# Performance work log

Measured on AMD Instinct MI355X. Metric: run time of the kernel, lower is better.

## Reference

```python
import jax, jax.numpy as jnp
import numpy as np
from jax import lax

C = 31  # channels (hyperspectral bands)
DN = ('NCHW', 'OIHW', 'NCHW')


def ln_bias(x, w, b):
    # WithBias LayerNorm over channel dim (torch does it in (b,hw,c) layout)
    mu = x.mean(axis=1, keepdims=True)
    var = x.var(axis=1, keepdims=True)
    xn = (x - mu) * lax.rsqrt(var + 1e-5)
    return xn * w[None, :, None, None] + b[None, :, None, None]


def conv1x1(x, W, b):
    y = lax.conv_general_dilated(x, W, (1, 1), 'VALID', dimension_numbers=DN)
    return y + b[None, :, None, None]


def dwconv3(x, W, b=None):
    c = x.shape[1]
    y = lax.conv_general_dilated(x, W, (1, 1), ((1, 1), (1, 1)),
                                 dimension_numbers=DN, feature_group_count=c)
    if b is not None:
        y = y + b[None, :, None, None]
    return y


def l2norm_lastdim(v):
    n = jnp.sqrt(jnp.sum(v * v, axis=-1, keepdims=True))
    return v / jnp.maximum(n, 1e-12)


def setup_inputs() -> dict:
    key = jax.random.key(0)
    ks = jax.random.split(key, 16)
    B, H, W = 4, 512, 512
    s = 0.05
    d = {
        'x': jax.random.normal(ks[0], (B, 1, H, W), jnp.float32),
        'z': jax.random.normal(ks[1], (B, C, H, W), jnp.float32),
        'nx_w': jnp.ones((1,), jnp.float32),
        'nx_b': jnp.zeros((1,), jnp.float32),
        'nz_w': jnp.ones((C,), jnp.float32),
        'nz_b': jnp.zeros((C,), jnp.float32),
        't1_w': jax.random.normal(ks[2], (C, C, 1, 1), jnp.float32) * s,
        't1_b': jnp.zeros((C,), jnp.float32),
        't2_w': jax.random.normal(ks[3], (C, 1, 3, 3), jnp.float32) * s,
        't2_b': jnp.zeros((C,), jnp.float32),
        'p1_w': jax.random.normal(ks[4], (C, 1, 1, 1), jnp.float32) * s,
        'p1_b': jnp.zeros((C,), jnp.float32),
        'p2_w': jax.random.normal(ks[5], (C, 1, 3, 3), jnp.float32) * s,
        'p2_b': jnp.zeros((C,), jnp.float32),
        'g1_w': jax.random.normal(ks[6], (C, C, 1, 1), jnp.float32) * s,
        'g1_b': jnp.zeros((C,), jnp.float32),
        'g2_w': jax.random.normal(ks[7], (C, 1, 3, 3), jnp.float32) * s,
        'g2_b': jnp.zeros((C,), jnp.float32),
        'w_w': jax.random.normal(ks[8], (C, C, 1, 1), jnp.float32) * s,
        'w_b': jnp.zeros((C,), jnp.float32),
        'v_w': jax.random.normal(ks[9], (C + 1, C + 1, 1, 1), jnp.float32) * s,
        'v_b': jnp.zeros((C + 1,), jnp.float32),
        'pe1_w': jax.random.normal(ks[10], (C, 1, 3, 3), jnp.float32) * s,
        'pe2_w': jax.random.normal(ks[11], (C, 1, 3, 3), jnp.float32) * s,
    }
    return d


def reference(x, z, nx_w, nx_b, nz_w, nz_b, t1_w, t1_b, t2_w, t2_b,
              p1_w, p1_b, p2_w, p2_b, g1_w, g1_b, g2_w, g2_b,
              w_w, w_b, v_w, v_b, pe1_w, pe2_w):
    b, _, h, w = x.shape
    x0 = ln_bias(x, nx_w, nx_b)            # (b,1,h,w)
    z0 = ln_bias(z, nz_w, nz_b)            # (b,C,h,w)

    z1 = dwconv3(conv1x1(z0, t1_w, t1_b), t2_w, t2_b).reshape(b, C, h * w)
    x1 = dwconv3(conv1x1(x0, p1_w, p1_b), p2_w, p2_b).reshape(b, C, h * w)

    z1 = l2norm_lastdim(z1)
    x1 = l2norm_lastdim(x1)

    att = jax.nn.softmax(jnp.einsum('bcn,bdn->bcd', z1, x1), axis=-1)  # (b,C,C)

    z2 = dwconv3(conv1x1(z0, g1_w, g1_b), g2_w, g2_b)  # (b,C,h,w)
    z_v = z2.reshape(b, C, h * w)
    out_x = jnp.einsum('bcd,bdn->bcn', att, z_v).reshape(b, C, h, w)

    pos = dwconv3(jax.nn.gelu(dwconv3(z2, pe1_w), approximate=False), pe2_w)
    out_x = conv1x1(out_x, w_w, w_b) + pos + z

    y = conv1x1(jnp.concatenate([x, out_x], axis=1), v_w, v_b)  # (b,C+1,h,w)
    return y
```

## Files before the change

kernel.cpp:

```cpp
#include <hip/hip_runtime.h>
#include <hip/hip_fp16.h>
#include <math.h>

#define BN 4
#define CC 31
#define HH 512
#define WW 512
#define HWSZ 262144

static const size_t Z2F = (size_t)BN * CC * HWSZ;
#define T_OFF   0
#define SSQ_OFF 124
#define R0_OFF  248
#define RL_OFF  372
#define C0_OFF  496
#define CL_OFF  620
#define COR_OFF 744
#define M2_OFF  1240
#define VB2_OFF 5208

typedef short v8s __attribute__((ext_vector_type(8)));
typedef _Float16 v8h __attribute__((ext_vector_type(8)));
typedef float v4f __attribute__((ext_vector_type(4)));
typedef _Float16 v4h __attribute__((ext_vector_type(4)));

__device__ __forceinline__ short f2bf(float f) {
    unsigned u = __float_as_uint(f);
    return (short)((u + 0x7FFFu + ((u >> 16) & 1u)) >> 16);
}

__device__ __forceinline__ float fast_gelu(float s) {
    const float a  = fabsf(s) * 0.70710678118654752f;
    const float t  = __builtin_amdgcn_rcpf(1.f + 0.3275911f * a);
    float p = 1.061405429f;
    p = p * t - 1.453152027f;
    p = p * t + 1.421413741f;
    p = p * t - 0.284496736f;
    p = p * t + 0.254829592f;
    const float e  = __expf(-a * a);
    const float er = copysignf(1.f - p * t * e, s);
    return 0.5f * s * (1.f + er);
}

__device__ __forceinline__ void swizzle_tile(int& b, int& ty0, int& tx0) {
    const int lid = blockIdx.x + 32 * blockIdx.y + 1024 * blockIdx.z;
    const int vid = ((lid & 7) << 9) + (lid >> 3);
    b = vid >> 10;
    const int rem = vid & 1023;
    ty0 = (rem >> 5) << 4;
    tx0 = (rem & 31) << 4;
}

__global__ __launch_bounds__(256, 4) void blockNL_k_stage1(
    const float* __restrict__ z,
    const float* __restrict__ nz_w, const float* __restrict__ nz_b,
    const float* __restrict__ t1w, const float* __restrict__ t1b,
    const float* __restrict__ t2w, const float* __restrict__ t2b,
    const float* __restrict__ g1w, const float* __restrict__ g1b,
    const float* __restrict__ g2w, const float* __restrict__ g2b,
    __half* __restrict__ z2out, float* __restrict__ stats)
{
    __shared__ __align__(16) short Vb[324 * 32];
    __shared__ __align__(16) short Wp[16 * 32];
    __shared__ __align__(16) short Ff[324 * 16];
    __shared__ __align__(16) short Zb[16 * 264];
    __shared__ __align__(16) short Wd[10 * 16];

    const int tid = threadIdx.x;
    int b, ty0, tx0;
    swizzle_tile(b, ty0, tx0);

    const int w = tid >> 6, lane = tid & 63, quad = lane >> 4, m15 = lane & 15;
    const int ty = tid >> 4, tx = tid & 15;
    const int gy = ty0 + ty, gx = tx0 + tx;

    for (int hp = tid; hp < 324; hp += 256) {
        const int hy = hp / 18, hx = hp - hy * 18;
        const int zy = ty0 + hy - 1, zx = tx0 + hx - 1;
        const bool valid = ((unsigned)zy < (unsigned)HH) && ((unsigned)zx < (unsigned)WW);
        int pk[16];
        if (valid) {
            const float* zp = z + (size_t)b * CC * HWSZ + (size_t)zy * WW + zx;
            float v[CC];
            float mu = 0.f;
            #pragma unroll
            for (int c = 0; c < CC; ++c) { v[c] = zp[(size_t)c * HWSZ]; mu += v[c]; }
            mu *= (1.f / 31.f);
            float var = 0.f;
            #pragma unroll
            for (int c = 0; c < CC; ++c) { float d = v[c] - mu; v[c] = d; var += d * d; }
            var *= (1.f / 31.f);
            const float rs = rsqrtf(var + 1e-5f);
            #pragma unroll
            for (int c = 0; c < CC; ++c) v[c] = v[c] * rs * nz_w[c] + nz_b[c];
            #pragma unroll
            for (int i = 0; i < 15; ++i)
                asm("v_cvt_pk_bf16_f32 %0, %1, %2"
                    : "=v"(pk[i]) : "v"(v[2 * i]), "v"(v[2 * i + 1]));
            asm("v_cvt_pk_bf16_f32 %0, %1, %2"
                : "=v"(pk[15]) : "v"(v[30]), "v"(0.f));
        } else {
            #pragma unroll
            for (int i = 0; i < 16; ++i) pk[i] = 0;
        }
        int* dst = (int*)&Vb[hp * 32];
        #pragma unroll
        for (int q = 0; q < 4; ++q) {
            int4 t; t.x = pk[q*4]; t.y = pk[q*4+1]; t.z = pk[q*4+2]; t.w = pk[q*4+3];
            ((int4*)dst)[q] = t;
        }
    }

    auto wbuild = [&](int p) {
        const float* W1 = (p >= 2) ? g1w : t1w;
        const int ct = p & 1;
        const int m = tid >> 4, kp = tid & 15;
        const int gr = ct * 16 + m;
        const int k0 = 2 * kp, k1 = k0 + 1;
        float w0 = 0.f, w1 = 0.f;
        if (gr < CC) {
            if (k0 < CC) w0 = W1[gr * CC + k0];
            if (k1 < CC) w1 = W1[gr * CC + k1];
        }
        ((int*)Wp)[m * 16 + kp] =
            (int)((unsigned short)f2bf(w0) | ((unsigned)(unsigned short)f2bf(w1) << 16));
    };

    auto wdbuild = [&](int p) {
        if (tid < 160) {
            const float* W3 = (p >= 2) ? g2w : t2w;
            const float* B3 = (p >= 2) ? g2b : t2b;
            const int tap = tid >> 4, r = tid & 15;
            const int ch = (p & 1) * 16 + r;
            float v = 0.f;
            if (ch < CC) v = (tap < 9) ? W3[ch * 9 + tap] : B3[ch];
            Wd[tap * 16 + r] = (short)__half_as_ushort(__float2half(v));
        }
    };

    auto mfma_pass = [&](int p) {
        const int ct = p & 1;
        const float* B1 = (p >= 2) ? g1b : t1b;
        const v8s afrag = *(const v8s*)&Wp[m15 * 32 + quad * 8];
        float bias[4];
        #pragma unroll
        for (int r = 0; r < 4; ++r) {
            const int row = ct * 16 + quad * 4 + r;
            bias[r] = (row < CC) ? B1[row] : 0.f;
        }
        for (int j = w; j < 21; j += 4) {
            const int px = j * 16 + m15;
            const int pc = (px < 324) ? px : 323;
            const v8s bfrag = *(const v8s*)&Vb[pc * 32 + quad * 8];
            v4f acc = {0.f, 0.f, 0.f, 0.f};
            acc = __builtin_amdgcn_mfma_f32_16x16x32_bf16(afrag, bfrag, acc, 0, 0, 0);
            if (px < 324) {
                unsigned d0 = (unsigned)__half_as_ushort(__float2half(acc[0] + bias[0]))
                            | ((unsigned)__half_as_ushort(__float2half(acc[1] + bias[1])) << 16);
                unsigned d1 = (unsigned)__half_as_ushort(__float2half(acc[2] + bias[2]))
                            | ((unsigned)__half_as_ushort(__float2half(acc[3] + bias[3])) << 16);
                const int half = (quad >> 1) ^ ((px >> 2) & 1);
                int2 st; st.x = (int)d0; st.y = (int)d1;
                *(int2*)&Ff[px * 16 + half * 8 + (quad & 1) * 4] = st;
            }
        }
    };

    auto dw3_pass = [&](int p) {
        const int ct = p & 1;
        const bool isG = (p >= 2);
        __half2 accv[8];
        {
            const v8s b0 = *(const v8s*)&Wd[9 * 16 + 0];
            const v8s b1 = *(const v8s*)&Wd[9 * 16 + 8];
            #pragma unroll
            for (int i = 0; i < 4; ++i) {
                accv[i]     = ((const __half2*)&b0)[i];
                accv[4 + i] = ((const __half2*)&b1)[i];
            }
        }
        #pragma unroll
        for (int dy = 0; dy < 3; ++dy)
            #pragma unroll
            for (int dx = 0; dx < 3; ++dx) {
                const int tap = dy * 3 + dx;
                const int hp = (ty + dy) * 18 + (tx + dx);
                const int sel = (hp >> 2) & 1;
                const v8s f0 = *(const v8s*)&Ff[hp * 16 + sel * 8];
                const v8s f1 = *(const v8s*)&Ff[hp * 16 + (sel ^ 1) * 8];
                const v8s w0 = *(const v8s*)&Wd[tap * 16 + 0];
                const v8s w1 = *(const v8s*)&Wd[tap * 16 + 8];
                #pragma unroll
                for (int i = 0; i < 4; ++i) {
                    accv[i]     = __hfma2(((const __half2*)&w0)[i],
                                          ((const __half2*)&f0)[i], accv[i]);
                    accv[4 + i] = __hfma2(((const __half2*)&w1)[i],
                                          ((const __half2*)&f1)[i], accv[4 + i]);
                }
            }
        if (isG) {
            const size_t zbase = (size_t)b * CC * HWSZ + (size_t)gy * WW + gx;
            #pragma unroll
            for (int i = 0; i < 8; ++i) {
                const unsigned u = *(const unsigned*)&accv[i];
                const int ch0 = ct * 16 + 2 * i, ch1 = ch0 + 1;
                z2out[zbase + (size_t)ch0 * HWSZ] =
                    __ushort_as_half((unsigned short)(u & 0xFFFFu));
                if (ch1 < CC)
                    z2out[zbase + (size_t)ch1 * HWSZ] =
                        __ushort_as_half((unsigned short)(u >> 16));
            }
        } else {
            #pragma unroll
            for (int i = 0; i < 8; ++i) {
                const unsigned u = *(const unsigned*)&accv[i];
                Zb[(2 * i) * 264 + tid]     = (short)(u & 0xFFFFu);
                Zb[(2 * i + 1) * 264 + tid] = (short)(u >> 16);
            }
            const bool top = (gy == 0), bot = (gy == HH - 1);
            const bool lef = (gx == 0), rig = (gx == WW - 1);
            if (top | bot | lef | rig) {
                #pragma unroll
                for (int r = 0; r < 16; ++r) {
                    const int ch = ct * 16 + r;
                    if (ch < CC) {
                        const unsigned u = *(const unsigned*)&accv[r >> 1];
                        const float sT = __half2float(__ushort_as_half(
                            (unsigned short)((r & 1) ? (u >> 16) : (u & 0xFFFFu))));
                        if (top) atomicAdd(&stats[R0_OFF + b * CC + ch], sT);
                        if (bot) atomicAdd(&stats[RL_OFF + b * CC + ch], sT);
                        if (lef) atomicAdd(&stats[C0_OFF + b * CC + ch], sT);
                        if (rig) atomicAdd(&stats[CL_OFF + b * CC + ch], sT);
                        if ((top || bot) && (lef || rig))
                            stats[COR_OFF + (b * CC + ch) * 4 +
                                  (bot ? 2 : 0) + (rig ? 1 : 0)] = sT;
                    }
                }
            }
        }
    };

    auto stats_pass = [&](int ct) {
        const bool dosq = (w >> 1);
        const int kh = w & 1;
        v8h onesh;
        #pragma unroll
        for (int i = 0; i < 8; ++i) onesh[i] = (_Float16)1.f;
        v4f acc = {0.f, 0.f, 0.f, 0.f};
        #pragma unroll
        for (int i = 0; i < 4; ++i) {
            const int ks = kh * 4 + i;
            const v8h bf = *(const v8h*)&Zb[m15 * 264 + ks * 32 + quad * 8];
            acc = __builtin_amdgcn_mfma_f32_16x16x32_f16(dosq ? bf : onesh, bf, acc, 0, 0, 0);
        }
        if (!dosq) {
            if (quad == 0) {
                const int ch = ct * 16 + m15;
                if (ch < CC) atomicAdd(&stats[T_OFF + b * CC + ch], acc[0]);
            }
        } else {
            if ((m15 >> 2) == quad) {
                const int r = m15 & 3;
                const int ch = ct * 16 + m15;
                if (ch < CC) atomicAdd(&stats[SSQ_OFF + b * CC + ch], acc[r]);
            }
        }
    };

    wbuild(0); wdbuild(0);
    __syncthreads();
    mfma_pass(0);
    __syncthreads();
    dw3_pass(0);
    __syncthreads();
    stats_pass(0); wbuild(1); wdbuild(1);
    __syncthreads();
    mfma_pass(1);
    __syncthreads();
    dw3_pass(1);
    __syncthreads();
    stats_pass(1); wbuild(2); wdbuild(2);
    __syncthreads();
    mfma_pass(2);
    __syncthreads();
    dw3_pass(2); wbuild(3);
    __syncthreads();
    mfma_pass(3); wdbuild(3);
    __syncthreads();
    dw3_pass(3);
}

__global__ void blockNL_k_att(
    const float* __restrict__ nx_b,
    const float* __restrict__ p1w, const float* __restrict__ p1b,
    const float* __restrict__ p2w, const float* __restrict__ p2b,
    const float* __restrict__ ww,  const float* __restrict__ wb,
    const float* __restrict__ vw,  const float* __restrict__ vb,
    float* stats)
{
    __shared__ float x1v[CC][9];
    __shared__ float dxs[CC];
    __shared__ float att[CC][CC];
    __shared__ float WA[CC][CC];

    const int tid = threadIdx.x;
    const int b = blockIdx.x;
    const float cnt[9] = {1.f, 510.f, 1.f, 510.f, 260100.f, 510.f, 1.f, 510.f, 1.f};

    if (tid < CC) {
        const float a = nx_b[0];
        const float u = p1w[tid] * a + p1b[tid];
        float w9[9];
        #pragma unroll
        for (int k = 0; k < 9; ++k) w9[k] = p2w[tid * 9 + k];
        float ssq = 0.f;
        #pragma unroll
        for (int ry = 0; ry < 3; ++ry) {
            #pragma unroll
            for (int rx = 0; rx < 3; ++rx) {
                float wsum = 0.f;
                #pragma unroll
                for (int ky = 0; ky < 3; ++ky) {
                    #pragma unroll
                    for (int kx = 0; kx < 3; ++kx) {
                        const bool okr = (ry == 1) || (ry == 0 && ky >= 1) || (ry == 2 && ky <= 1);
                        const bool okc = (rx == 1) || (rx == 0 && kx >= 1) || (rx == 2 && kx <= 1);
                        if (okr && okc) wsum += w9[ky * 3 + kx];
                    }
                }
                const float val = u * wsum + p2b[tid];
                x1v[tid][ry * 3 + rx] = val;
                ssq += cnt[ry * 3 + rx] * val * val;
            }
        }
        dxs[tid] = fmaxf(sqrtf(ssq), 1e-12f);
    }
    if (b == 0 && tid < 32) {
        float s = vb[tid];
        #pragma unroll
        for (int c = 0; c < CC; ++c) s += vw[tid * 32 + c + 1] * wb[c];
        stats[VB2_OFF + tid] = s;
    }
    __syncthreads();

    if (tid < CC) {
        const int c = tid;
        const float Tt  = stats[T_OFF  + b * CC + c];
        const float sq  = stats[SSQ_OFF + b * CC + c];
        const float r0  = stats[R0_OFF + b * CC + c];
        const float rL  = stats[RL_OFF + b * CC + c];
        const float c0  = stats[C0_OFF + b * CC + c];
        const float cL  = stats[CL_OFF + b * CC + c];
        const float k00 = stats[COR_OFF + (b * CC + c) * 4 + 0];
        const float k01 = stats[COR_OFF + (b * CC + c) * 4 + 1];
        const float k10 = stats[COR_OFF + (b * CC + c) * 4 + 2];
        const float k11 = stats[COR_OFF + (b * CC + c) * 4 + 3];
        float T[9];
        T[0] = k00; T[2] = k01; T[6] = k10; T[8] = k11;
        T[1] = r0 - k00 - k01;
        T[7] = rL - k10 - k11;
        T[3] = c0 - k00 - k10;
        T[5] = cL - k01 - k11;
        T[4] = Tt - r0 - rL - c0 - cL + k00 + k01 + k10 + k11;
        const float dz = fmaxf(sqrtf(sq), 1e-12f);

        float Arow[CC];
        float mx = -3.4e38f;
        #pragma unroll
        for (int d = 0; d < CC; ++d) {
            float s = 0.f;
            #pragma unroll
            for (int r = 0; r < 9; ++r) s += T[r] * x1v[d][r];
            s = s / (dz * dxs[d]);
            Arow[d] = s;
            mx = fmaxf(mx, s);
        }
        float den = 0.f;
        #pragma unroll
        for (int d = 0; d < CC; ++d) { float e = expf(Arow[d] - mx); Arow[d] = e; den += e; }
        const float inv = 1.f / den;
        #pragma unroll
        for (int d = 0; d < CC; ++d) att[c][d] = Arow[d] * inv;
    }
    __syncthreads();
    if (tid < CC) {
        const int c2 = tid;
        #pragma unroll
        for (int d = 0; d < CC; ++d) {
            float s = 0.f;
            #pragma unroll
            for (int c = 0; c < CC; ++c) s += ww[c2 * CC + c] * att[c][d];
            WA[c2][d] = s;
        }
    }
    __syncthreads();
    if (tid < 32) {
        const int e = tid;
        #pragma unroll
        for (int d = 0; d < CC; ++d) {
            float s = 0.f;
            #pragma unroll
            for (int c2 = 0; c2 < CC; ++c2) s += vw[e * 32 + c2 + 1] * WA[c2][d];
            stats[M2_OFF + (b * 32 + e) * CC + d] = s;
        }
    }
}

__global__ __launch_bounds__(256, 4) void blockNL_k_out(
    const float* __restrict__ x, const float* __restrict__ z,
    const float* __restrict__ vw,
    const float* __restrict__ pe1w, const float* __restrict__ pe2w,
    const __half* __restrict__ z2, const float* __restrict__ stats,
    float* __restrict__ out)
{
    __shared__ float zb[8][408];
    __shared__ float qb[8][328];
    __shared__ __align__(16) short Ub[256 * 20];
    __shared__ __align__(16) short A2[4 * 32 * 20];

    const int tid = threadIdx.x;
    int b, ty0, tx0;
    swizzle_tile(b, ty0, tx0);
    const int ty = tid >> 4, tx = tid & 15;
    const int gy = ty0 + ty, gx = tx0 + tx;

    const float* M2 = stats + M2_OFF + b * 32 * CC;
    for (int idx = tid; idx < 2048; idx += 256) {
        const int ci = idx >> 9, e = (idx >> 4) & 31, k = idx & 15;
        const int ch = ci * 8 + (k & 7);
        float v = 0.f;
        if (ch < 31) v = (k < 8) ? vw[e * 32 + 1 + ch] : M2[e * CC + ch];
        A2[(ci * 32 + e) * 20 + k] = (short)__half_as_ushort(__float2half(v));
    }

    const int w = tid >> 6, lane = tid & 63, quad = lane >> 4, m15 = lane & 15;
    const int mt = w & 1, jbase = (w >> 1) * 8;
    const size_t zpix = (size_t)b * CC * HWSZ + (size_t)gy * WW + gx;

    int  gzo[6];
    bool gvv[6];
    #pragma unroll
    for (int k = 0; k < 6; ++k) {
        const int p = lane + 64 * k;
        const int hy = p / 18, hx = p - hy * 18;
        const bool inr = (p < 324);
        gzo[k] = inr ? (hy * 20 + hx) : 0;
        gvv[k] = inr && ((unsigned)(ty0 + hy - 1) < (unsigned)HH) &&
                 ((unsigned)(tx0 + hx - 1) < (unsigned)WW);
    }
    const bool sact = (tid < 200);
    const int shy = tid / 10, shx2 = (tid - shy * 10) * 2;
    const int szy = ty0 + shy - 2, szx = tx0 + shx2 - 2;
    const bool sv = sact && ((unsigned)szy < (unsigned)HH) &&
                    ((unsigned)szx < (unsigned)WW);
    const long sgoff = (long)szy * WW + szx;
    const int zwo = shy * 20 + shx2;

    v4f acc[8];
    #pragma unroll
    for (int jj = 0; jj < 8; ++jj) acc[jj] = (v4f){0.f, 0.f, 0.f, 0.f};

    auto stage = [&](int ci) {
        const unsigned short* z2u = (const unsigned short*)z2;
        #pragma unroll
        for (int c8 = 0; c8 < 8; ++c8) {
            const int ch = ci * 8 + c8;
            float2 f = {0.f, 0.f};
            if (sv && ch < 31) {
                const unsigned word = *(const unsigned*)(z2u +
                    (size_t)(b * CC + ch) * HWSZ + sgoff);
                f = __half22float2(*(const __half2*)&word);
            }
            if (sact) *(float2*)&zb[c8][zwo] = f;
        }
    };

    stage(0);

    for (int ci = 0; ci < 4; ++ci) {
        __syncthreads();
        #pragma unroll
        for (int j = 0; j < 2; ++j) {
            const int cc = 2 * w + j;
            const int ch = ci * 8 + cc;
            float wv[9];
            #pragma unroll
            for (int k = 0; k < 9; ++k) wv[k] = (ch < 31) ? pe1w[ch * 9 + k] : 0.f;
            #pragma unroll
            for (int k = 0; k < 6; ++k) {
                const int p = lane + 64 * k;
                if (k < 5 || p < 324) {
                    float q = 0.f;
                    if (gvv[k]) {
                        float s = 0.f;
                        #pragma unroll
                        for (int dy = 0; dy < 3; ++dy)
                            #pragma unroll
                            for (int dx = 0; dx < 3; ++dx)
                                s += wv[dy * 3 + dx] * zb[cc][gzo[k] + dy * 20 + dx];
                        q = fast_gelu(s);
                    }
                    qb[cc][p] = q;
                }
            }
        }
        __syncthreads();
        {
            unsigned pk[8];
            #pragma unroll
            for (int r = 0; r < 8; ++r) {
                const int ch = ci * 8 + r;
                float tval = 0.f, zval = 0.f;
                if (ch < 31) {
                    float pos = 0.f;
                    #pragma unroll
                    for (int dy = 0; dy < 3; ++dy)
                        #pragma unroll
                        for (int dx = 0; dx < 3; ++dx)
                            pos += pe2w[ch * 9 + dy * 3 + dx] * qb[r][(ty + dy) * 18 + (tx + dx)];
                    tval = pos + z[zpix + (size_t)ch * HWSZ];
                    zval = zb[r][(ty + 2) * 20 + (tx + 2)];
                }
                pk[r] = (unsigned)__half_as_ushort(__float2half(tval))
                      | ((unsigned)__half_as_ushort(__float2half(zval)) << 16);
            }
            int* ub = (int*)&Ub[tid * 20];
            int2 s0, s1, s2, s3;
            s0.x = (int)((pk[0] & 0xFFFFu) | (pk[1] << 16));
            s0.y = (int)((pk[2] & 0xFFFFu) | (pk[3] << 16));
            s1.x = (int)((pk[4] & 0xFFFFu) | (pk[5] << 16));
            s1.y = (int)((pk[6] & 0xFFFFu) | (pk[7] << 16));
            s2.x = (int)((pk[0] >> 16) | (pk[1] & 0xFFFF0000u));
            s2.y = (int)((pk[2] >> 16) | (pk[3] & 0xFFFF0000u));
            s3.x = (int)((pk[4] >> 16) | (pk[5] & 0xFFFF0000u));
            s3.y = (int)((pk[6] >> 16) | (pk[7] & 0xFFFF0000u));
            ((int2*)ub)[0] = s0;
            ((int2*)ub)[1] = s1;
            ((int2*)ub)[2] = s2;
            ((int2*)ub)[3] = s3;
        }
        __syncthreads();
        {
            const v4h a = *(const v4h*)&A2[(ci * 32 + mt * 16 + m15) * 20 + quad * 4];
            #pragma unroll
            for (int jj = 0; jj < 8; ++jj) {
                const int p = (jbase + jj) * 16 + m15;
                const v4h bv = *(const v4h*)&Ub[p * 20 + quad * 4];
                acc[jj] = __builtin_amdgcn_mfma_f32_16x16x16f16(a, bv, acc[jj], 0, 0, 0);
            }
        }
        if (ci < 3) stage(ci + 1);
    }

    {
        float vb2r[4], vw0[4];
        #pragma unroll
        for (int r = 0; r < 4; ++r) {
            const int e = mt * 16 + quad * 4 + r;
            vb2r[r] = stats[VB2_OFF + e];
            vw0[r]  = vw[e * 32];
        }
        #pragma unroll
        for (int jj = 0; jj < 8; ++jj) {
            const int p = (jbase + jj) * 16 + m15;
            const int py = p >> 4, px = p & 15;
            const int ogy = ty0 + py, ogx = tx0 + px;
            const float xv = x[(size_t)b * HWSZ + (size_t)ogy * WW + ogx];
            const size_t obase = (size_t)b * 32 * HWSZ + (size_t)ogy * WW + ogx;
            #pragma unroll
            for (int r = 0; r < 4; ++r) {
                const int e = mt * 16 + quad * 4 + r;
                out[obase + (size_t)e * HWSZ] = acc[jj][r] + vb2r[r] + vw0[r] * xv;
            }
        }
    }
}

extern "C" void kernel_launch(void* const* d_in, const int* in_sizes, int n_in,
                              void* d_out, int out_size, void* d_ws, size_t ws_size,
                              hipStream_t stream)
{
    (void)in_sizes; (void)n_in; (void)out_size; (void)ws_size;

    const float* x    = (const float*)d_in[0];
    const float* z    = (const float*)d_in[1];
    const float* nx_b = (const float*)d_in[3];
    const float* nz_w = (const float*)d_in[4];
    const float* nz_b = (const float*)d_in[5];
    const float* t1w  = (const float*)d_in[6];
    const float* t1b  = (const float*)d_in[7];
    const float* t2w  = (const float*)d_in[8];
    const float* t2b  = (const float*)d_in[9];
    const float* p1w  = (const float*)d_in[10];
    const float* p1b  = (const float*)d_in[11];
    const float* p2w  = (const float*)d_in[12];
    const float* p2b  = (const float*)d_in[13];
    const float* g1w  = (const float*)d_in[14];
    const float* g1b  = (const float*)d_in[15];
    const float* g2w  = (const float*)d_in[16];
    const float* g2b  = (const float*)d_in[17];
    const float* ww   = (const float*)d_in[18];
    const float* wb   = (const float*)d_in[19];
    const float* vw   = (const float*)d_in[20];
    const float* vb   = (const float*)d_in[21];
    const float* pe1w = (const float*)d_in[22];
    const float* pe2w = (const float*)d_in[23];

    __half* z2   = (__half*)d_ws;
    float* stats = (float*)((char*)d_ws + Z2F * sizeof(__half));

    hipMemsetAsync(stats, 0, 1240 * sizeof(float), stream);

    dim3 grid(WW / 16, HH / 16, BN);
    dim3 blk(256);

    blockNL_k_stage1<<<grid, blk, 0, stream>>>(z, nz_w, nz_b, t1w, t1b, t2w, t2b,
                                               g1w, g1b, g2w, g2b, z2, stats);
    blockNL_k_att<<<4, 64, 0, stream>>>(nx_b, p1w, p1b, p2w, p2b, ww, wb, vw, vb,
                                        stats);
    blockNL_k_out<<<grid, blk, 0, stream>>>(x, z, vw, pe1w, pe2w, z2, stats,
                                            (float*)d_out);
}
```

Before: 603.4 us.

## Use packed half2 math and half shared buffers for positional depthwise convs

Keeps the staged z2 tile and the GELU intermediate in shared memory as packed fp16 channel pairs instead of fp32. Both depthwise 3x3 convolutions now run with __hfma2 on two channels at once, using pre-packed half2 weights held in shared memory. This halves LDS footprint and traffic and the FMA count in the out kernel, which may raise occupancy. In exchange, the conv accumulations are done in fp16, which loses precision.

New measurement: 567.3 us. 6.0% less time.

```diff
diff --git a/kernel.cpp b/kernel.cpp
--- a/kernel.cpp
+++ b/kernel.cpp
@@ -413,10 +413,12 @@
     const __half* __restrict__ z2, const float* __restrict__ stats,
     float* __restrict__ out)
 {
-    __shared__ float zb[8][408];
-    __shared__ float qb[8][328];
+    __shared__ __align__(16) unsigned zb2[4][400];
+    __shared__ __align__(16) unsigned qb2[4][324];
     __shared__ __align__(16) short Ub[256 * 20];
     __shared__ __align__(16) short A2[4 * 32 * 20];
+    __shared__ unsigned W1h[144];
+    __shared__ unsigned W2h[144];
 
     const int tid = threadIdx.x;
     int b, ty0, tx0;
@@ -431,6 +433,19 @@
         float v = 0.f;
         if (ch < 31) v = (k < 8) ? vw[e * 32 + 1 + ch] : M2[e * CC + ch];
         A2[(ci * 32 + e) * 20 + k] = (short)__half_as_ushort(__float2half(v));
+    }
+    for (int idx = tid; idx < 288; idx += 256) {
+        const int t = (idx >= 144);
+        const int r = idx - t * 144;
+        const int ci = r / 36, rem = r - ci * 36;
+        const int tap = rem >> 2, pr = rem & 3;
+        const int ch0 = ci * 8 + 2 * pr, ch1 = ch0 + 1;
+        const float* Ws = t ? pe2w : pe1w;
+        const float a = Ws[ch0 * 9 + tap];
+        const float bb = (ch1 < 31) ? Ws[ch1 * 9 + tap] : 0.f;
+        const unsigned u = (unsigned)__half_as_ushort(__float2half(a))
+                         | ((unsigned)__half_as_ushort(__float2half(bb)) << 16);
+        (t ? W2h : W1h)[r] = u;
     }
 
     const int w = tid >> 6, lane = tid & 63, quad = lane >> 4, m15 = lane & 15;
@@ -463,15 +478,20 @@
     auto stage = [&](int ci) {
         const unsigned short* z2u = (const unsigned short*)z2;
         #pragma unroll
-        for (int c8 = 0; c8 < 8; ++c8) {
-            const int ch = ci * 8 + c8;
-            float2 f = {0.f, 0.f};
-            if (sv && ch < 31) {
-                const unsigned word = *(const unsigned*)(z2u +
-                    (size_t)(b * CC + ch) * HWSZ + sgoff);
-                f = __half22float2(*(const __half2*)&word);
-            }
-            if (sact) *(float2*)&zb[c8][zwo] = f;
+        for (int pr = 0; pr < 4; ++pr) {
+            const int ch0 = ci * 8 + 2 * pr, ch1 = ch0 + 1;
+            unsigned wa = 0, wb = 0;
+            if (sv) {
+                wa = *(const unsigned*)(z2u + (size_t)(b * CC + ch0) * HWSZ + sgoff);
+                if (ch1 < 31)
+                    wb = *(const unsigned*)(z2u + (size_t)(b * CC + ch1) * HWSZ + sgoff);
+            }
+            const unsigned u0 = (wa & 0xFFFFu) | (wb << 16);
+            const unsigned u1 = (wa >> 16) | (wb & 0xFFFF0000u);
+            if (sact) {
+                uint2 st; st.x = u0; st.y = u1;
+                *(uint2*)&zb2[pr][zwo] = st;
+            }
         }
     };
 
@@ -479,61 +499,71 @@
 
     for (int ci = 0; ci < 4; ++ci) {
         __syncthreads();
-        #pragma unroll
-        for (int j = 0; j < 2; ++j) {
-            const int cc = 2 * w + j;
-            const int ch = ci * 8 + cc;
-            float wv[9];
-            #pragma unroll
-            for (int k = 0; k < 9; ++k) wv[k] = (ch < 31) ? pe1w[ch * 9 + k] : 0.f;
+        {
+            const int pr = w;
+            unsigned wv2[9];
+            #pragma unroll
+            for (int t = 0; t < 9; ++t) wv2[t] = W1h[ci * 36 + t * 4 + pr];
             #pragma unroll
             for (int k = 0; k < 6; ++k) {
                 const int p = lane + 64 * k;
                 if (k < 5 || p < 324) {
-                    float q = 0.f;
+                    unsigned qo = 0;
                     if (gvv[k]) {
-                        float s = 0.f;
+                        __half2 s2h = __float2half2_rn(0.f);
                         #pragma unroll
                         for (int dy = 0; dy < 3; ++dy)
                             #pragma unroll
                             for (int dx = 0; dx < 3; ++dx)
-                                s += wv[dy * 3 + dx] * zb[cc][gzo[k] + dy * 20 + dx];
-                        q = fast_gelu(s);
+                                s2h = __hfma2(*(const __half2*)&wv2[dy * 3 + dx],
+                                              *(const __half2*)&zb2[pr][gzo[k] + dy * 20 + dx],
+                                              s2h);
+                        const float2 f = __half22float2(s2h);
+                        const float q0 = fast_gelu(f.x), q1 = fast_gelu(f.y);
+                        qo = (unsigned)__half_as_ushort(__float2half(q0))
+                           | ((unsigned)__half_as_ushort(__float2half(q1)) << 16);
                     }
-                    qb[cc][p] = q;
+                    qb2[pr][p] = qo;
                 }
             }
         }
         __syncthreads();
         {
-            unsigned pk[8];
-            #pragma unroll
-            for (int r = 0; r < 8; ++r) {
-                const int ch = ci * 8 + r;
-                float tval = 0.f, zval = 0.f;
-                if (ch < 31) {
-                    float pos = 0.f;
+            __half2 pos2[4];
+            #pragma unroll
+            for (int pr = 0; pr < 4; ++pr) pos2[pr] = __float2half2_rn(0.f);
+            #pragma unroll
+            for (int dy = 0; dy < 3; ++dy)
+                #pragma unroll
+                for (int dx = 0; dx < 3; ++dx) {
+                    const int tap = dy * 3 + dx;
+                    const int qoff = (ty + dy) * 18 + (tx + dx);
                     #pragma unroll
-                    for (int dy = 0; dy < 3; ++dy)
-                        #pragma unroll
-                        for (int dx = 0; dx < 3; ++dx)
-                            pos += pe2w[ch * 9 + dy * 3 + dx] * qb[r][(ty + dy) * 18 + (tx + dx)];
-                    tval = pos + z[zpix + (size_t)ch * HWSZ];
-                    zval = zb[r][(ty + 2) * 20 + (tx + 2)];
+                    for (int pr = 0; pr < 4; ++pr) {
+                        const unsigned wq = W2h[ci * 36 + tap * 4 + pr];
+                        pos2[pr] = __hfma2(*(const __half2*)&wq,
+                                           *(const __half2*)&qb2[pr][qoff], pos2[pr]);
+                    }
                 }
-                pk[r] = (unsigned)__half_as_ushort(__float2half(tval))
-                      | ((unsigned)__half_as_ushort(__float2half(zval)) << 16);
+            unsigned tpk[4], zc[4];
+            const int ctr = (ty + 2) * 20 + (tx + 2);
+            #pragma unroll
+            for (int pr = 0; pr < 4; ++pr) {
+                zc[pr] = zb2[pr][ctr];
+                const int ch0 = ci * 8 + 2 * pr, ch1 = ch0 + 1;
+                const float2 pf = __half22float2(pos2[pr]);
+                const float t0 = pf.x + z[zpix + (size_t)ch0 * HWSZ];
+                float t1 = 0.f;
+                if (ch1 < 31) t1 = pf.y + z[zpix + (size_t)ch1 * HWSZ];
+                tpk[pr] = (unsigned)__half_as_ushort(__float2half(t0))
+                        | ((unsigned)__half_as_ushort(__float2half(t1)) << 16);
             }
             int* ub = (int*)&Ub[tid * 20];
             int2 s0, s1, s2, s3;
-            s0.x = (int)((pk[0] & 0xFFFFu) | (pk[1] << 16));
-            s0.y = (int)((pk[2] & 0xFFFFu) | (pk[3] << 16));
-            s1.x = (int)((pk[4] & 0xFFFFu) | (pk[5] << 16));
-            s1.y = (int)((pk[6] & 0xFFFFu) | (pk[7] << 16));
-            s2.x = (int)((pk[0] >> 16) | (pk[1] & 0xFFFF0000u));
-            s2.y = (int)((pk[2] >> 16) | (pk[3] & 0xFFFF0000u));
-            s3.x = (int)((pk[4] >> 16) | (pk[5] & 0xFFFF0000u));
-            s3.y = (int)((pk[6] >> 16) | (pk[7] & 0xFFFF0000u));
+            s0.x = (int)tpk[0]; s0.y = (int)tpk[1];
+            s1.x = (int)tpk[2]; s1.y = (int)tpk[3];
+            s2.x = (int)zc[0];  s2.y = (int)zc[1];
+            s3.x = (int)zc[2];  s3.y = (int)zc[3];
             ((int2*)ub)[0] = s0;
             ((int2*)ub)[1] = s1;
             ((int2*)ub)[2] = s2;
```
